# Performance work log

Measured on AMD Instinct MI355X. Metric: run time of the kernel, lower is better.

The kernel has to match this reference:

```python
import jax, jax.numpy as jnp
import numpy as np

N_NODES = 50000
N_EDGES = 800000
D_IN = 128
H1 = 128
H2 = 64
N_CLASSES = 4


def _sage_conv(x, src, dst, w_l, w_r, b, num_nodes):
    # PyG SAGEConv (aggr='mean'): out = lin_l(mean_{j->i} x_j) + lin_r(x_i)
    ones = jnp.ones((src.shape[0],), dtype=x.dtype)
    deg = jax.ops.segment_sum(ones, dst, num_segments=num_nodes)  # [N]
    agg = jax.ops.segment_sum(x[src], dst, num_segments=num_nodes)  # [N, d]
    agg = agg / jnp.maximum(deg, 1.0)[:, None]
    return agg @ w_l + b + x @ w_r


def setup_inputs() -> dict:
    key = jax.random.key(0)
    ks = jax.random.split(key, 12)
    x_content = jax.random.normal(ks[0], (N_NODES, D_IN), dtype=jnp.float32)
    edge_index = jax.random.randint(ks[1], (2, N_EDGES), 0, N_NODES, dtype=jnp.int32)
    edge_type = jax.random.randint(ks[2], (N_EDGES,), 0, 4, dtype=jnp.int32)
    s = 0.05
    params = {
        'w_l0': jax.random.normal(ks[3], (D_IN, H1), jnp.float32) * s,
        'w_r0': jax.random.normal(ks[4], (D_IN, H1), jnp.float32) * s,
        'b0': jnp.zeros((H1,), jnp.float32),
        'w_l1': jax.random.normal(ks[5], (H1, H1), jnp.float32) * s,
        'w_r1': jax.random.normal(ks[6], (H1, H1), jnp.float32) * s,
        'b1': jnp.zeros((H1,), jnp.float32),
        'w_l2': jax.random.normal(ks[7], (H1, H2), jnp.float32) * s,
        'w_r2': jax.random.normal(ks[8], (H1, H2), jnp.float32) * s,
        'b2': jnp.zeros((H2,), jnp.float32),
        'w_out': jax.random.normal(ks[9], (H2, N_CLASSES), jnp.float32) * s,
        'b_out': jnp.zeros((N_CLASSES,), jnp.float32),
    }
    return {'x_content': x_content, 'edge_index': edge_index, 'edge_type': edge_type, **params}


def reference(x_content, edge_index, edge_type,
              w_l0, w_r0, b0, w_l1, w_r1, b1, w_l2, w_r2, b2, w_out, b_out):
    # eval mode: dropout is identity
    src, dst = edge_index[0], edge_index[1]
    n = x_content.shape[0]
    x = x_content
    for (wl, wr, b) in ((w_l0, w_r0, b0), (w_l1, w_r1, b1), (w_l2, w_r2, b2)):
        x = _sage_conv(x, src, dst, wl, wr, b, n)
        x = jax.nn.relu(x)
    return x @ w_out + b_out
```

## Files before the change

### kernel.cpp

```cpp
#include <hip/hip_runtime.h>
#include <hip/hip_fp16.h>

#define D 128

constexpr int NRANGE = 8;
constexpr int NCHUNK = 32;
constexpr int RRC = 6272;

using short8 = __attribute__((ext_vector_type(8))) short;
using f32x4 = __attribute__((ext_vector_type(4))) float;

__device__ inline void splitf(float v, unsigned short& h, unsigned short& l) {
    unsigned b = __float_as_uint(v);
    h = (unsigned short)(b >> 16);
    float fh = __uint_as_float(b & 0xffff0000u);
    float r = v - fh;
    l = (unsigned short)(__float_as_uint(r) >> 16);
}


__global__ __launch_bounds__(1024) void hist_count(
    const int* __restrict__ dst, int* __restrict__ hist,
    int n_edges, int n_nodes, int rr, int ch) {
    __shared__ int lh[RRC];
    int b = blockIdx.x;
    int r = b & (NRANGE - 1), c = b >> 3;
    int t = threadIdx.x;
    for (int i = t; i < rr; i += 1024) lh[i] = 0;
    __syncthreads();
    int lo = r * rr, hi = min(n_nodes, lo + rr);
    int e0 = c * ch, e1 = min(n_edges, e0 + ch);
    for (int e = e0 + t; e < e1; e += 1024) {
        int d = dst[e];
        if (d >= lo && d < hi) atomicAdd(&lh[d - lo], 1);
    }
    __syncthreads();
    int* gh = hist + (size_t)(r * NCHUNK + c) * rr;
    for (int i = t; i < rr; i += 1024) gh[i] = lh[i];
}

__global__ __launch_bounds__(256) void deg_sum_partials(
    const int* __restrict__ hist, int* __restrict__ deg,
    int* __restrict__ partials, int n_nodes, int rr) {
    __shared__ int sd[256];
    int b = blockIdx.x, t = threadIdx.x;
    int i = b * 256 + t;
    int s = 0;
    if (i < n_nodes) {
        int r = i / rr, ii = i - r * rr;
        for (int c = 0; c < NCHUNK; ++c) s += hist[(size_t)(r * NCHUNK + c) * rr + ii];
        deg[i] = s;
    }
    sd[t] = s;
    __syncthreads();
    for (int st = 128; st > 0; st >>= 1) {
        if (t < st) sd[t] += sd[t + st];
        __syncthreads();
    }
    if (t == 0) partials[b] = sd[0];
}

__global__ __launch_bounds__(256) void scan_fill(
    const int* __restrict__ deg, const int* __restrict__ partials,
    const int* __restrict__ hist, int* __restrict__ row_ptr,
    float* __restrict__ inv_deg, int* __restrict__ base,
    int n_nodes, int rr, int nblk) {
    __shared__ int sp[256];
    __shared__ int sd[256];
    int b = blockIdx.x, t = threadIdx.x;

    sp[t] = (t < b && t < nblk) ? partials[t] : 0;
    __syncthreads();
    for (int st = 128; st > 0; st >>= 1) {
        if (t < st) sp[t] += sp[t + st];
        __syncthreads();
    }
    int pbase = sp[0];

    int i = b * 256 + t;
    int v = (i < n_nodes) ? deg[i] : 0;
    sd[t] = v;
    __syncthreads();
    for (int d = 1; d < 256; d <<= 1) {
        int x = (t >= d) ? sd[t - d] : 0;
        __syncthreads();
        sd[t] += x;
        __syncthreads();
    }
    int excl = sd[t] - v + pbase;
    if (i < n_nodes) {
        row_ptr[i] = excl;
        int dv = v > 1 ? v : 1;
        inv_deg[i] = 1.0f / (float)dv;
        if (i == n_nodes - 1) row_ptr[n_nodes] = excl + v;
        int r = i / rr, ii = i - r * rr;
        int bacc = excl;
        for (int c = 0; c < NCHUNK; ++c) {
            size_t idx = (size_t)(r * NCHUNK + c) * rr + ii;
            base[idx] = bacc;
            bacc += hist[idx];
        }
    }
}

__global__ __launch_bounds__(1024) void fill_part(
    const int* __restrict__ src, const int* __restrict__ dst,
    const int* __restrict__ base, int* __restrict__ csr,
    int n_edges, int n_nodes, int rr, int ch) {
    __shared__ int cur[RRC];
    int b = blockIdx.x;
    int r = b & (NRANGE - 1), c = b >> 3;
    int t = threadIdx.x;
    const int* gb = base + (size_t)(r * NCHUNK + c) * rr;
    for (int i = t; i < rr; i += 1024) cur[i] = gb[i];
    __syncthreads();
    int lo = r * rr, hi = min(n_nodes, lo + rr);
    int e0 = c * ch, e1 = min(n_edges, e0 + ch);
    for (int e = e0 + t; e < e1; e += 1024) {
        int d = dst[e];
        if (d >= lo && d < hi) {
            int slot = atomicAdd(&cur[d - lo], 1);
            csr[slot] = src[e];
        }
    }
}

struct WSplitArgs {
    const float* src[6];
    unsigned short* dh[6];
    unsigned short* dl[6];
    int n[6];
};

__global__ __launch_bounds__(256) void split_w(WSplitArgs a) {
    int m = blockIdx.y;
    int N = a.n[m];
    int e = blockIdx.x * 256 + threadIdx.x;
    if (e >= 128 * N) return;
    int sh = (N == 128) ? 7 : 6;
    int k = e >> sh;
    int n = e & (N - 1);
    float v = a.src[m][e];
    unsigned short h, l;
    splitf(v, h, l);
    a.dh[m][n * 128 + k] = h;
    a.dl[m][n * 128 + k] = l;
}

template <int BN, int NT, bool SPLITX>
__global__ __launch_bounds__(256) void gemm_lds(
    const float* __restrict__ X,
    const unsigned short* __restrict__ Ah, const unsigned short* __restrict__ Al,
    const unsigned short* __restrict__ W1h, const unsigned short* __restrict__ W1l,
    const unsigned short* __restrict__ W2h, const unsigned short* __restrict__ W2l,
    const float* __restrict__ bias, __half* __restrict__ P, float* __restrict__ Q, int M) {
    __shared__ short8 As[2][16 * 65];

    const int tid = threadIdx.x;
    const int wave = tid >> 6;
    const int lane = tid & 63;
    const int l15 = lane & 15;
    const int q = lane >> 4;
    const int m0 = blockIdx.x * 64;

    if constexpr (SPLITX) {
#pragma unroll
        for (int it = 0; it < 4; ++it) {
            int s = it * 256 + tid;
            int row = s >> 4, col16 = s & 15;
            int gr = min(m0 + row, M - 1);
            const float4* xp = (const float4*)X + (size_t)gr * 32 + col16 * 2;
            float4 v0 = xp[0], v1 = xp[1];
            float fv[8] = {v0.x, v0.y, v0.z, v0.w, v1.x, v1.y, v1.z, v1.w};
            short8 h, l;
#pragma unroll
            for (int j = 0; j < 8; ++j) {
                unsigned short hh_, ll_;
                splitf(fv[j], hh_, ll_);
                h[j] = (short)hh_;
                l[j] = (short)ll_;
            }
            As[0][col16 * 65 + row] = h;
            As[1][col16 * 65 + row] = l;
        }
    } else {
#pragma unroll
        for (int it = 0; it < 8; ++it) {
            int s = it * 256 + tid;
            int arr = s >> 10;
            int sp = s & 1023;
            int row = sp >> 4, col16 = sp & 15;
            int gr = min(m0 + row, M - 1);
            const unsigned short* src = (arr ? Al : Ah) + (size_t)gr * 128 + col16 * 8;
            As[arr][col16 * 65 + row] = *(const short8*)src;
        }
    }
    __syncthreads();

    const int isQ = wave >> 1;
    const int colbase = (wave & 1) * (NT * 16);
    const unsigned short* Wh = isQ ? W2h : W1h;
    const unsigned short* Wl = isQ ? W2l : W1l;

    float bvs[NT];
#pragma unroll
    for (int nt = 0; nt < NT; ++nt) bvs[nt] = isQ ? bias[colbase + nt * 16 + l15] : 0.f;

    f32x4 acc[4][NT] = {};

#pragma unroll 1
    for (int kt = 0; kt < 4; ++kt) {
        short8 Bh[NT], Bl[NT];
#pragma unroll
        for (int nt = 0; nt < NT; ++nt) {
            int c = colbase + nt * 16 + l15;
            int off = c * 128 + kt * 32 + q * 8;
            Bh[nt] = *(const short8*)(Wh + off);
            Bl[nt] = *(const short8*)(Wl + off);
        }
#pragma unroll
        for (int mt = 0; mt < 4; ++mt) {
            int ai = (kt * 4 + q) * 65 + mt * 16 + l15;
            short8 Afh = As[0][ai];
            short8 Afl = As[1][ai];
#pragma unroll
            for (int nt = 0; nt < NT; ++nt) {
                acc[mt][nt] = __builtin_amdgcn_mfma_f32_16x16x32_bf16(Afh, Bh[nt], acc[mt][nt], 0, 0, 0);
                acc[mt][nt] = __builtin_amdgcn_mfma_f32_16x16x32_bf16(Afh, Bl[nt], acc[mt][nt], 0, 0, 0);
                acc[mt][nt] = __builtin_amdgcn_mfma_f32_16x16x32_bf16(Afl, Bh[nt], acc[mt][nt], 0, 0, 0);
            }
        }
    }

#pragma unroll
    for (int mt = 0; mt < 4; ++mt) {
        int orow = m0 + mt * 16 + q * 4;
#pragma unroll
        for (int nt = 0; nt < NT; ++nt) {
            int col = colbase + nt * 16 + l15;
#pragma unroll
            for (int r = 0; r < 4; ++r) {
                int rr = orow + r;
                if (rr < M) {
                    if (isQ) Q[(size_t)rr * BN + col] = acc[mt][nt][r] + bvs[nt];
                    else P[(size_t)rr * BN + col] = __float2half(acc[mt][nt][r]);
                }
            }
        }
    }
}

__global__ __launch_bounds__(256) void agg_fused128(
    const __half* __restrict__ P, const float* __restrict__ Q,
    const int* __restrict__ row_ptr, const int* __restrict__ csr,
    const float* __restrict__ inv_deg, unsigned short* __restrict__ Hh,
    unsigned short* __restrict__ Hl, int n_nodes) {
    int node = (blockIdx.x * blockDim.x + threadIdx.x) >> 6;
    int lane = threadIdx.x & 63;
    if (node >= n_nodes) return;
    int beg = row_ptr[node], end = row_ptr[node + 1];
    const int g = lane >> 4;
    const int l = lane & 15;
    float a[2][8] = {};
    int e = beg;
    for (; e + 8 <= end; e += 8) {
#pragma unroll
        for (int j = 0; j < 2; ++j) {
            int s = csr[e + 4 * j + g];
            uint4 raw = *(const uint4*)(P + (size_t)s * 128 + l * 8);
            float2 f01 = __half22float2(*reinterpret_cast<__half2*>(&raw.x));
            float2 f23 = __half22float2(*reinterpret_cast<__half2*>(&raw.y));
            float2 f45 = __half22float2(*reinterpret_cast<__half2*>(&raw.z));
            float2 f67 = __half22float2(*reinterpret_cast<__half2*>(&raw.w));
            a[j][0] += f01.x; a[j][1] += f01.y; a[j][2] += f23.x; a[j][3] += f23.y;
            a[j][4] += f45.x; a[j][5] += f45.y; a[j][6] += f67.x; a[j][7] += f67.y;
        }
    }
    for (; e < end; e += 4) {
        int idx = e + g;
        if (idx < end) {
            int s = csr[idx];
            uint4 raw = *(const uint4*)(P + (size_t)s * 128 + l * 8);
            float2 f01 = __half22float2(*reinterpret_cast<__half2*>(&raw.x));
            float2 f23 = __half22float2(*reinterpret_cast<__half2*>(&raw.y));
            float2 f45 = __half22float2(*reinterpret_cast<__half2*>(&raw.z));
            float2 f67 = __half22float2(*reinterpret_cast<__half2*>(&raw.w));
            a[0][0] += f01.x; a[0][1] += f01.y; a[0][2] += f23.x; a[0][3] += f23.y;
            a[0][4] += f45.x; a[0][5] += f45.y; a[0][6] += f67.x; a[0][7] += f67.y;
        }
    }
    float s[8];
#pragma unroll
    for (int k = 0; k < 8; ++k) {
        s[k] = a[0][k] + a[1][k];
        s[k] += __shfl_xor(s[k], 16);
        s[k] += __shfl_xor(s[k], 32);
    }
    if (lane < 16) {
        float w = inv_deg[node];
        const float4* Q4 = (const float4*)Q;
        float4 q0 = Q4[(size_t)node * 32 + 2 * l];
        float4 q1 = Q4[(size_t)node * 32 + 2 * l + 1];
        float h0 = fmaxf(fmaf(s[0], w, q0.x), 0.f);
        float h1 = fmaxf(fmaf(s[1], w, q0.y), 0.f);
        float h2 = fmaxf(fmaf(s[2], w, q0.z), 0.f);
        float h3 = fmaxf(fmaf(s[3], w, q0.w), 0.f);
        float h4 = fmaxf(fmaf(s[4], w, q1.x), 0.f);
        float h5 = fmaxf(fmaf(s[5], w, q1.y), 0.f);
        float h6 = fmaxf(fmaf(s[6], w, q1.z), 0.f);
        float h7 = fmaxf(fmaf(s[7], w, q1.w), 0.f);
        ushort4 hv0, lv0, hv1, lv1;
        splitf(h0, hv0.x, lv0.x);
        splitf(h1, hv0.y, lv0.y);
        splitf(h2, hv0.z, lv0.z);
        splitf(h3, hv0.w, lv0.w);
        splitf(h4, hv1.x, lv1.x);
        splitf(h5, hv1.y, lv1.y);
        splitf(h6, hv1.z, lv1.z);
        splitf(h7, hv1.w, lv1.w);
        ((ushort4*)Hh)[(size_t)node * 32 + 2 * l] = hv0;
        ((ushort4*)Hh)[(size_t)node * 32 + 2 * l + 1] = hv1;
        ((ushort4*)Hl)[(size_t)node * 32 + 2 * l] = lv0;
        ((ushort4*)Hl)[(size_t)node * 32 + 2 * l + 1] = lv1;
    }
}

__global__ __launch_bounds__(256) void agg64_head(
    const __half* __restrict__ P, const float* __restrict__ Q,
    const int* __restrict__ row_ptr, const int* __restrict__ csr,
    const float* __restrict__ inv_deg, const float* __restrict__ Wo,
    const float* __restrict__ bo, float* __restrict__ out, int n_nodes) {
    int node = (blockIdx.x * blockDim.x + threadIdx.x) >> 6;
    int lane = threadIdx.x & 63;
    if (node >= n_nodes) return;
    int beg = row_ptr[node], end = row_ptr[node + 1];
    const int quarter = lane >> 4;
    const int l = lane & 15;
    float a[2][4] = {};
    int e = beg;
    for (; e + 8 <= end; e += 8) {
#pragma unroll
        for (int j = 0; j < 2; ++j) {
            int s = csr[e + 4 * j + quarter];
            uint2 raw = *(const uint2*)(P + (size_t)s * 64 + l * 4);
            float2 f01 = __half22float2(*reinterpret_cast<__half2*>(&raw.x));
            float2 f23 = __half22float2(*reinterpret_cast<__half2*>(&raw.y));
            a[j][0] += f01.x; a[j][1] += f01.y; a[j][2] += f23.x; a[j][3] += f23.y;
        }
    }
    for (; e < end; e += 4) {
        int idx = e + quarter;
        if (idx < end) {
            int s = csr[idx];
            uint2 raw = *(const uint2*)(P + (size_t)s * 64 + l * 4);
            float2 f01 = __half22float2(*reinterpret_cast<__half2*>(&raw.x));
            float2 f23 = __half22float2(*reinterpret_cast<__half2*>(&raw.y));
            a[0][0] += f01.x; a[0][1] += f01.y; a[0][2] += f23.x; a[0][3] += f23.y;
        }
    }
    float s0 = a[0][0] + a[1][0];
    float s1 = a[0][1] + a[1][1];
    float s2 = a[0][2] + a[1][2];
    float s3 = a[0][3] + a[1][3];
    s0 += __shfl_xor(s0, 16); s0 += __shfl_xor(s0, 32);
    s1 += __shfl_xor(s1, 16); s1 += __shfl_xor(s1, 32);
    s2 += __shfl_xor(s2, 16); s2 += __shfl_xor(s2, 32);
    s3 += __shfl_xor(s3, 16); s3 += __shfl_xor(s3, 32);
    if (lane < 16) {
        float w = inv_deg[node];
        float4 qv = ((const float4*)Q)[(size_t)node * 16 + l];
        float h0 = fmaxf(fmaf(s0, w, qv.x), 0.f);
        float h1 = fmaxf(fmaf(s1, w, qv.y), 0.f);
        float h2 = fmaxf(fmaf(s2, w, qv.z), 0.f);
        float h3 = fmaxf(fmaf(s3, w, qv.w), 0.f);
        const float4* Wo4 = (const float4*)Wo;
        float4 w0 = Wo4[4 * l + 0], w1 = Wo4[4 * l + 1], w2 = Wo4[4 * l + 2], w3 = Wo4[4 * l + 3];
        float c0 = h0 * w0.x + h1 * w1.x + h2 * w2.x + h3 * w3.x;
        float c1 = h0 * w0.y + h1 * w1.y + h2 * w2.y + h3 * w3.y;
        float c2 = h0 * w0.z + h1 * w1.z + h2 * w2.z + h3 * w3.z;
        float c3 = h0 * w0.w + h1 * w1.w + h2 * w2.w + h3 * w3.w;
#pragma unroll
        for (int m = 8; m > 0; m >>= 1) {
            c0 += __shfl_xor(c0, m);
            c1 += __shfl_xor(c1, m);
            c2 += __shfl_xor(c2, m);
            c3 += __shfl_xor(c3, m);
        }
        if (l == 0) {
            float4 r;
            r.x = c0 + bo[0];
            r.y = c1 + bo[1];
            r.z = c2 + bo[2];
            r.w = c3 + bo[3];
            ((float4*)out)[node] = r;
        }
    }
}

extern "C" void kernel_launch(void* const* d_in, const int* in_sizes, int n_in,
                              void* d_out, int out_size, void* d_ws, size_t ws_size,
                              hipStream_t stream) {
    const float* x = (const float*)d_in[0];
    const int* ei = (const int*)d_in[1];
    const float* wl0 = (const float*)d_in[3];
    const float* wr0 = (const float*)d_in[4];
    const float* b0 = (const float*)d_in[5];
    const float* wl1 = (const float*)d_in[6];
    const float* wr1 = (const float*)d_in[7];
    const float* b1 = (const float*)d_in[8];
    const float* wl2 = (const float*)d_in[9];
    const float* wr2 = (const float*)d_in[10];
    const float* b2 = (const float*)d_in[11];
    const float* wo = (const float*)d_in[12];
    const float* bo = (const float*)d_in[13];

    const int n_nodes = in_sizes[0] / D;
    const int n_edges = in_sizes[1] / 2;
    const int* srcp = ei;
    const int* dstp = ei + n_edges;

    char* ws = (char*)d_ws;
    size_t off = 0;
    auto carve = [&](size_t bytes) -> void* {
        void* p = ws + off;
        off = (off + bytes + 255) & ~(size_t)255;
        return p;
    };
    int* deg = (int*)carve((size_t)n_nodes * 4);
    int* row_ptr = (int*)carve((size_t)(n_nodes + 1) * 4);
    int* partials = (int*)carve(256 * 4);
    float* inv_deg = (float*)carve((size_t)n_nodes * 4);
    int* csr = (int*)carve((size_t)n_edges * 4);
    __half* Pbuf = (__half*)carve((size_t)n_nodes * D * 2);
    float* Qbuf = (float*)carve((size_t)n_nodes * D * 4);
    unsigned short* hh = (unsigned short*)carve((size_t)n_nodes * D * 2);
    unsigned short* hl = (unsigned short*)carve((size_t)n_nodes * D * 2);
    unsigned short* wt = (unsigned short*)carve((size_t)(4 * 128 * 128 + 2 * 64 * 128) * 2 * 2);
    unsigned short* wl0h = wt;
    unsigned short* wl0l = wl0h + 128 * 128;
    unsigned short* wr0h = wl0l + 128 * 128;
    unsigned short* wr0l = wr0h + 128 * 128;
    unsigned short* wl1h = wr0l + 128 * 128;
    unsigned short* wl1l = wl1h + 128 * 128;
    unsigned short* wr1h = wl1l + 128 * 128;
    unsigned short* wr1l = wr1h + 128 * 128;
    unsigned short* wl2h = wr1l + 128 * 128;
    unsigned short* wl2l = wl2h + 64 * 128;
    unsigned short* wr2h = wl2l + 64 * 128;
    unsigned short* wr2l = wr2h + 64 * 128;

    const int rr = (n_nodes + NRANGE - 1) / NRANGE;
    const int ch = (n_edges + NCHUNK - 1) / NCHUNK;
    int* hist = (int*)Qbuf;
    int* basep = (int*)Pbuf;

    const int nblk = (n_nodes + 255) / 256;

    hist_count<<<NRANGE * NCHUNK, 1024, 0, stream>>>(dstp, hist, n_edges, n_nodes, rr, ch);
    deg_sum_partials<<<nblk, 256, 0, stream>>>(hist, deg, partials, n_nodes, rr);
    scan_fill<<<nblk, 256, 0, stream>>>(deg, partials, hist, row_ptr, inv_deg, basep, n_nodes, rr, nblk);
    fill_part<<<NRANGE * NCHUNK, 1024, 0, stream>>>(srcp, dstp, basep, csr, n_edges, n_nodes, rr, ch);

    WSplitArgs wa;
    wa.src[0] = wl0; wa.dh[0] = wl0h; wa.dl[0] = wl0l; wa.n[0] = 128;
    wa.src[1] = wr0; wa.dh[1] = wr0h; wa.dl[1] = wr0l; wa.n[1] = 128;
    wa.src[2] = wl1; wa.dh[2] = wl1h; wa.dl[2] = wl1l; wa.n[2] = 128;
    wa.src[3] = wr1; wa.dh[3] = wr1h; wa.dl[3] = wr1l; wa.n[3] = 128;
    wa.src[4] = wl2; wa.dh[4] = wl2h; wa.dl[4] = wl2l; wa.n[4] = 64;
    wa.src[5] = wr2; wa.dh[5] = wr2h; wa.dl[5] = wr2l; wa.n[5] = 64;
    split_w<<<dim3(64, 6), 256, 0, stream>>>(wa);

    const int agg_blocks = (n_nodes * 64 + 255) / 256;
    const int gemm_blocks = (n_nodes + 63) / 64;

    gemm_lds<128, 4, true><<<gemm_blocks, 256, 0, stream>>>(
        x, nullptr, nullptr, wl0h, wl0l, wr0h, wr0l, b0, Pbuf, Qbuf, n_nodes);
    agg_fused128<<<agg_blocks, 256, 0, stream>>>(Pbuf, Qbuf, row_ptr, csr, inv_deg, hh, hl, n_nodes);
    gemm_lds<128, 4, false><<<gemm_blocks, 256, 0, stream>>>(
        nullptr, hh, hl, wl1h, wl1l, wr1h, wr1l, b1, Pbuf, Qbuf, n_nodes);
    agg_fused128<<<agg_blocks, 256, 0, stream>>>(Pbuf, Qbuf, row_ptr, csr, inv_deg, hh, hl, n_nodes);
    gemm_lds<64, 2, false><<<gemm_blocks, 256, 0, stream>>>(
        nullptr, hh, hl, wl2h, wl2l, wr2h, wr2l, b2, Pbuf, Qbuf, n_nodes);
    agg64_head<<<agg_blocks, 256, 0, stream>>>(Pbuf, Qbuf, row_ptr, csr, inv_deg,
                                               wo, bo, (float*)d_out, n_nodes);
}
```

Before: 306.7 us.

## Fuse neighbor aggregation into next-layer GEMM and rank-based CSR fill

The mean-aggregation kernel is fused into the following layer's split-bf16 MFMA GEMM. Each block aggregates its 64 nodes directly into LDS instead of writing hi/lo activation buffers to global memory and reading them back, and P/Q are double-buffered across layers. CSR construction now records a per-edge rank during the histogram pass using packed 16-bit LDS counters, so the fill becomes a simple per-edge scatter without a second atomic pass. The weight split is folded into the degree-sum kernel to save a launch. In exchange, the fused kernel runs only 4 waves per 64-node tile for the irregular gather, which may cut the parallelism available to hide latency.

```diff
diff --git a/kernel.cpp b/kernel.cpp
--- a/kernel.cpp
+++ b/kernel.cpp
@@ -3,9 +3,11 @@
 
 #define D 128
 
-constexpr int NRANGE = 8;
-constexpr int NCHUNK = 32;
-constexpr int RRC = 6272;
+constexpr int RSH = 14;
+constexpr int RSZ = 1 << RSH;
+constexpr int NRANGE = 4;
+constexpr int CSH = 15;
+constexpr int CSZ = 1 << CSH;
 
 using short8 = __attribute__((ext_vector_type(8))) short;
 using f32x4 = __attribute__((ext_vector_type(4))) float;
@@ -19,36 +21,62 @@
 }
 
 
-__global__ __launch_bounds__(1024) void hist_count(
-    const int* __restrict__ dst, int* __restrict__ hist,
-    int n_edges, int n_nodes, int rr, int ch) {
-    __shared__ int lh[RRC];
+__global__ __launch_bounds__(1024) void hist_rank(
+    const int* __restrict__ dst, unsigned* __restrict__ hist,
+    unsigned short* __restrict__ rank, int n_edges, int nchunk) {
+    __shared__ unsigned lh[RSZ / 2];
     int b = blockIdx.x;
-    int r = b & (NRANGE - 1), c = b >> 3;
+    int r = b & (NRANGE - 1), c = b >> 2;
     int t = threadIdx.x;
-    for (int i = t; i < rr; i += 1024) lh[i] = 0;
-    __syncthreads();
-    int lo = r * rr, hi = min(n_nodes, lo + rr);
-    int e0 = c * ch, e1 = min(n_edges, e0 + ch);
+    for (int i = t; i < RSZ / 2; i += 1024) lh[i] = 0;
+    __syncthreads();
+    int e0 = c << CSH, e1 = min(n_edges, e0 + CSZ);
     for (int e = e0 + t; e < e1; e += 1024) {
         int d = dst[e];
-        if (d >= lo && d < hi) atomicAdd(&lh[d - lo], 1);
-    }
-    __syncthreads();
-    int* gh = hist + (size_t)(r * NCHUNK + c) * rr;
-    for (int i = t; i < rr; i += 1024) gh[i] = lh[i];
-}
-
-__global__ __launch_bounds__(256) void deg_sum_partials(
-    const int* __restrict__ hist, int* __restrict__ deg,
-    int* __restrict__ partials, int n_nodes, int rr) {
+        if ((d >> RSH) == r) {
+            int ii = d & (RSZ - 1);
+            unsigned sh = (ii & 1) * 16;
+            unsigned old = atomicAdd(&lh[ii >> 1], 1u << sh);
+            rank[e] = (unsigned short)((old >> sh) & 0xffffu);
+        }
+    }
+    __syncthreads();
+    unsigned* gh = hist + (size_t)(r * nchunk + c) * (RSZ / 2);
+    for (int i = t; i < RSZ / 2; i += 1024) gh[i] = lh[i];
+}
+
+struct WSplitArgs {
+    const float* src[6];
+    unsigned short* dh[6];
+    unsigned short* dl[6];
+};
+
+__global__ __launch_bounds__(256) void deg_splitw(
+    const unsigned short* __restrict__ hist16, int* __restrict__ deg,
+    int* __restrict__ partials, int n_nodes, int nchunk, int nblk, WSplitArgs a) {
     __shared__ int sd[256];
     int b = blockIdx.x, t = threadIdx.x;
+    if (b >= nblk) {
+        int g = (b - nblk) * 256 + t;
+        int m, e, N;
+        if (g < 65536) { m = g >> 14; e = g & 16383; N = 128; }
+        else { int t2 = g - 65536; m = 4 + (t2 >> 13); e = t2 & 8191; N = 64; }
+        int sh = (N == 128) ? 7 : 6;
+        int k = e >> sh;
+        int n = e & (N - 1);
+        float v = a.src[m][e];
+        unsigned short h, l;
+        splitf(v, h, l);
+        a.dh[m][n * 128 + k] = h;
+        a.dl[m][n * 128 + k] = l;
+        return;
+    }
     int i = b * 256 + t;
     int s = 0;
     if (i < n_nodes) {
-        int r = i / rr, ii = i - r * rr;
-        for (int c = 0; c < NCHUNK; ++c) s += hist[(size_t)(r * NCHUNK + c) * rr + ii];
+        int r = i >> RSH, ii = i & (RSZ - 1);
+        const unsigned short* hp = hist16 + (size_t)r * nchunk * RSZ + ii;
+        for (int c = 0; c < nchunk; ++c) s += hp[(size_t)c * RSZ];
         deg[i] = s;
     }
     sd[t] = s;
@@ -62,9 +90,9 @@
 
 __global__ __launch_bounds__(256) void scan_fill(
     const int* __restrict__ deg, const int* __restrict__ partials,
-    const int* __restrict__ hist, int* __restrict__ row_ptr,
+    const unsigned short* __restrict__ hist16, int* __restrict__ row_ptr,
     float* __restrict__ inv_deg, int* __restrict__ base,
-    int n_nodes, int rr, int nblk) {
+    int n_nodes, int nchunk, int nblk) {
     __shared__ int sp[256];
     __shared__ int sd[256];
     int b = blockIdx.x, t = threadIdx.x;
@@ -93,64 +121,31 @@
         int dv = v > 1 ? v : 1;
         inv_deg[i] = 1.0f / (float)dv;
         if (i == n_nodes - 1) row_ptr[n_nodes] = excl + v;
-        int r = i / rr, ii = i - r * rr;
+        int r = i >> RSH, ii = i & (RSZ - 1);
         int bacc = excl;
-        for (int c = 0; c < NCHUNK; ++c) {
-            size_t idx = (size_t)(r * NCHUNK + c) * rr + ii;
+        for (int c = 0; c < nchunk; ++c) {
+            size_t idx = (size_t)(r * nchunk + c) * RSZ + ii;
             base[idx] = bacc;
-            bacc += hist[idx];
-        }
-    }
-}
-
-__global__ __launch_bounds__(1024) void fill_part(
+            bacc += hist16[idx];
+        }
+    }
+}
+
+__global__ __launch_bounds__(256) void fill_edges(
     const int* __restrict__ src, const int* __restrict__ dst,
-    const int* __restrict__ base, int* __restrict__ csr,
-    int n_edges, int n_nodes, int rr, int ch) {
-    __shared__ int cur[RRC];
-    int b = blockIdx.x;
-    int r = b & (NRANGE - 1), c = b >> 3;
-    int t = threadIdx.x;
-    const int* gb = base + (size_t)(r * NCHUNK + c) * rr;
-    for (int i = t; i < rr; i += 1024) cur[i] = gb[i];
-    __syncthreads();
-    int lo = r * rr, hi = min(n_nodes, lo + rr);
-    int e0 = c * ch, e1 = min(n_edges, e0 + ch);
-    for (int e = e0 + t; e < e1; e += 1024) {
-        int d = dst[e];
-        if (d >= lo && d < hi) {
-            int slot = atomicAdd(&cur[d - lo], 1);
-            csr[slot] = src[e];
-        }
-    }
-}
-
-struct WSplitArgs {
-    const float* src[6];
-    unsigned short* dh[6];
-    unsigned short* dl[6];
-    int n[6];
-};
-
-__global__ __launch_bounds__(256) void split_w(WSplitArgs a) {
-    int m = blockIdx.y;
-    int N = a.n[m];
+    const unsigned short* __restrict__ rank, const int* __restrict__ base,
+    int* __restrict__ csr, int n_edges, int nchunk) {
     int e = blockIdx.x * 256 + threadIdx.x;
-    if (e >= 128 * N) return;
-    int sh = (N == 128) ? 7 : 6;
-    int k = e >> sh;
-    int n = e & (N - 1);
-    float v = a.src[m][e];
-    unsigned short h, l;
-    splitf(v, h, l);
-    a.dh[m][n * 128 + k] = h;
-    a.dl[m][n * 128 + k] = l;
-}
-
-template <int BN, int NT, bool SPLITX>
-__global__ __launch_bounds__(256) void gemm_lds(
+    if (e >= n_edges) return;
+    int d = dst[e];
+    int c = e >> CSH;
+    int r = d >> RSH;
+    int slot = base[(size_t)(r * nchunk + c) * RSZ + (d & (RSZ - 1))] + rank[e];
+    csr[slot] = src[e];
+}
+
+__global__ __launch_bounds__(256) void gemm_x(
     const float* __restrict__ X,
-    const unsigned short* __restrict__ Ah, const unsigned short* __restrict__ Al,
     const unsigned short* __restrict__ W1h, const unsigned short* __restrict__ W1l,
     const unsigned short* __restrict__ W2h, const unsigned short* __restrict__ W2l,
     const float* __restrict__ bias, __half* __restrict__ P, float* __restrict__ Q, int M) {
@@ -163,36 +158,166 @@
     const int q = lane >> 4;
     const int m0 = blockIdx.x * 64;
 
-    if constexpr (SPLITX) {
-#pragma unroll
-        for (int it = 0; it < 4; ++it) {
-            int s = it * 256 + tid;
-            int row = s >> 4, col16 = s & 15;
-            int gr = min(m0 + row, M - 1);
-            const float4* xp = (const float4*)X + (size_t)gr * 32 + col16 * 2;
-            float4 v0 = xp[0], v1 = xp[1];
-            float fv[8] = {v0.x, v0.y, v0.z, v0.w, v1.x, v1.y, v1.z, v1.w};
-            short8 h, l;
-#pragma unroll
-            for (int j = 0; j < 8; ++j) {
-                unsigned short hh_, ll_;
-                splitf(fv[j], hh_, ll_);
-                h[j] = (short)hh_;
-                l[j] = (short)ll_;
-            }
-            As[0][col16 * 65 + row] = h;
-            As[1][col16 * 65 + row] = l;
-        }
-    } else {
-#pragma unroll
-        for (int it = 0; it < 8; ++it) {
-            int s = it * 256 + tid;
-            int arr = s >> 10;
-            int sp = s & 1023;
-            int row = sp >> 4, col16 = sp & 15;
-            int gr = min(m0 + row, M - 1);
-            const unsigned short* src = (arr ? Al : Ah) + (size_t)gr * 128 + col16 * 8;
-            As[arr][col16 * 65 + row] = *(const short8*)src;
+#pragma unroll
+    for (int it = 0; it < 4; ++it) {
+        int s = it * 256 + tid;
+        int row = s >> 4, col16 = s & 15;
+        int gr = min(m0 + row, M - 1);
+        const float4* xp = (const float4*)X + (size_t)gr * 32 + col16 * 2;
+        float4 v0 = xp[0], v1 = xp[1];
+        float fv[8] = {v0.x, v0.y, v0.z, v0.w, v1.x, v1.y, v1.z, v1.w};
+        short8 h, l;
+#pragma unroll
+        for (int j = 0; j < 8; ++j) {
+            unsigned short hh_, ll_;
+            splitf(fv[j], hh_, ll_);
+            h[j] = (short)hh_;
+            l[j] = (short)ll_;
+        }
+        As[0][col16 * 65 + row] = h;
+        As[1][col16 * 65 + row] = l;
+    }
+    __syncthreads();
+
+    const int isQ = wave >> 1;
+    const int colbase = (wave & 1) * 64;
+    const unsigned short* Wh = isQ ? W2h : W1h;
+    const unsigned short* Wl = isQ ? W2l : W1l;
+
+    float bvs[4];
+#pragma unroll
+    for (int nt = 0; nt < 4; ++nt) bvs[nt] = isQ ? bias[colbase + nt * 16 + l15] : 0.f;
+
+    f32x4 acc[4][4] = {};
+
+#pragma unroll 1
+    for (int kt = 0; kt < 4; ++kt) {
+        short8 Bh[4], Bl[4];
+#pragma unroll
+        for (int nt = 0; nt < 4; ++nt) {
+            int c = colbase + nt * 16 + l15;
+            int off = c * 128 + kt * 32 + q * 8;
+            Bh[nt] = *(const short8*)(Wh + off);
+            Bl[nt] = *(const short8*)(Wl + off);
+        }
+#pragma unroll
+        for (int mt = 0; mt < 4; ++mt) {
+            int ai = (kt * 4 + q) * 65 + mt * 16 + l15;
+            short8 Afh = As[0][ai];
+            short8 Afl = As[1][ai];
+#pragma unroll
+            for (int nt = 0; nt < 4; ++nt) {
+                acc[mt][nt] = __builtin_amdgcn_mfma_f32_16x16x32_bf16(Afh, Bh[nt], acc[mt][nt], 0, 0, 0);
+                acc[mt][nt] = __builtin_amdgcn_mfma_f32_16x16x32_bf16(Afh, Bl[nt], acc[mt][nt], 0, 0, 0);
+                acc[mt][nt] = __builtin_amdgcn_mfma_f32_16x16x32_bf16(Afl, Bh[nt], acc[mt][nt], 0, 0, 0);
+            }
+        }
+    }
+
+#pragma unroll
+    for (int mt = 0; mt < 4; ++mt) {
+        int orow = m0 + mt * 16 + q * 4;
+#pragma unroll
+        for (int nt = 0; nt < 4; ++nt) {
+            int col = colbase + nt * 16 + l15;
+#pragma unroll
+            for (int r = 0; r < 4; ++r) {
+                int rr = orow + r;
+                if (rr < M) {
+                    if (isQ) Q[(size_t)rr * 128 + col] = acc[mt][nt][r] + bvs[nt];
+                    else P[(size_t)rr * 128 + col] = __float2half(acc[mt][nt][r]);
+                }
+            }
+        }
+    }
+}
+
+template <int BN, int NT>
+__global__ __launch_bounds__(256) void agg_gemm(
+    const __half* __restrict__ Pprev, const float* __restrict__ Qprev,
+    const int* __restrict__ row_ptr, const int* __restrict__ csr,
+    const float* __restrict__ inv_deg,
+    const unsigned short* __restrict__ W1h, const unsigned short* __restrict__ W1l,
+    const unsigned short* __restrict__ W2h, const unsigned short* __restrict__ W2l,
+    const float* __restrict__ bias, __half* __restrict__ P, float* __restrict__ Q, int M) {
+    __shared__ short8 As[2][16 * 65];
+
+    const int tid = threadIdx.x;
+    const int wave = tid >> 6;
+    const int lane = tid & 63;
+    const int l15 = lane & 15;
+    const int q = lane >> 4;
+    const int m0 = blockIdx.x * 64;
+
+#pragma unroll 1
+    for (int i = 0; i < 16; ++i) {
+        int row = (wave << 4) + i;
+        int node = m0 + row;
+        bool valid = node < M;
+        float a[2][8] = {};
+        if (valid) {
+            int beg = row_ptr[node], end = row_ptr[node + 1];
+            int e = beg;
+            for (; e + 8 <= end; e += 8) {
+#pragma unroll
+                for (int j = 0; j < 2; ++j) {
+                    int s = csr[e + 4 * j + q];
+                    uint4 raw = *(const uint4*)(Pprev + (size_t)s * 128 + l15 * 8);
+                    float2 f01 = __half22float2(*reinterpret_cast<__half2*>(&raw.x));
+                    float2 f23 = __half22float2(*reinterpret_cast<__half2*>(&raw.y));
+                    float2 f45 = __half22float2(*reinterpret_cast<__half2*>(&raw.z));
+                    float2 f67 = __half22float2(*reinterpret_cast<__half2*>(&raw.w));
+                    a[j][0] += f01.x; a[j][1] += f01.y; a[j][2] += f23.x; a[j][3] += f23.y;
+                    a[j][4] += f45.x; a[j][5] += f45.y; a[j][6] += f67.x; a[j][7] += f67.y;
+                }
+            }
+            for (; e < end; e += 4) {
+                int idx = e + q;
+                if (idx < end) {
+                    int s = csr[idx];
+                    uint4 raw = *(const uint4*)(Pprev + (size_t)s * 128 + l15 * 8);
+                    float2 f01 = __half22float2(*reinterpret_cast<__half2*>(&raw.x));
+                    float2 f23 = __half22float2(*reinterpret_cast<__half2*>(&raw.y));
+                    float2 f45 = __half22float2(*reinterpret_cast<__half2*>(&raw.z));
+                    float2 f67 = __half22float2(*reinterpret_cast<__half2*>(&raw.w));
+                    a[0][0] += f01.x; a[0][1] += f01.y; a[0][2] += f23.x; a[0][3] += f23.y;
+                    a[0][4] += f45.x; a[0][5] += f45.y; a[0][6] += f67.x; a[0][7] += f67.y;
+                }
+            }
+        }
+        float s8[8];
+#pragma unroll
+        for (int k = 0; k < 8; ++k) {
+            s8[k] = a[0][k] + a[1][k];
+            s8[k] += __shfl_xor(s8[k], 16);
+            s8[k] += __shfl_xor(s8[k], 32);
+        }
+        if (lane < 16) {
+            short8 h8 = {}, l8 = {};
+            if (valid) {
+                float w = inv_deg[node];
+                const float4* Q4 = (const float4*)Qprev;
+                float4 q0 = Q4[(size_t)node * 32 + 2 * l15];
+                float4 q1 = Q4[(size_t)node * 32 + 2 * l15 + 1];
+                float hv[8];
+                hv[0] = fmaxf(fmaf(s8[0], w, q0.x), 0.f);
+                hv[1] = fmaxf(fmaf(s8[1], w, q0.y), 0.f);
+                hv[2] = fmaxf(fmaf(s8[2], w, q0.z), 0.f);
+                hv[3] = fmaxf(fmaf(s8[3], w, q0.w), 0.f);
+                hv[4] = fmaxf(fmaf(s8[4], w, q1.x), 0.f);
+                hv[5] = fmaxf(fmaf(s8[5], w, q1.y), 0.f);
+                hv[6] = fmaxf(fmaf(s8[6], w, q1.z), 0.f);
+                hv[7] = fmaxf(fmaf(s8[7], w, q1.w), 0.f);
+#pragma unroll
+                for (int k = 0; k < 8; ++k) {
+                    unsigned short hh_, ll_;
+                    splitf(hv[k], hh_, ll_);
+                    h8[k] = (short)hh_;
+                    l8[k] = (short)ll_;
+                }
+            }
+            As[0][l15 * 65 + row] = h8;
+            As[1][l15 * 65 + row] = l8;
         }
     }
     __syncthreads();
@@ -247,81 +372,6 @@
                 }
             }
         }
-    }
-}
-
-__global__ __launch_bounds__(256) void agg_fused128(
-    const __half* __restrict__ P, const float* __restrict__ Q,
-    const int* __restrict__ row_ptr, const int* __restrict__ csr,
-    const float* __restrict__ inv_deg, unsigned short* __restrict__ Hh,
-    unsigned short* __restrict__ Hl, int n_nodes) {
-    int node = (blockIdx.x * blockDim.x + threadIdx.x) >> 6;
-    int lane = threadIdx.x & 63;
-    if (node >= n_nodes) return;
-    int beg = row_ptr[node], end = row_ptr[node + 1];
-    const int g = lane >> 4;
-    const int l = lane & 15;
-    float a[2][8] = {};
-    int e = beg;
-    for (; e + 8 <= end; e += 8) {
-#pragma unroll
-        for (int j = 0; j < 2; ++j) {
-            int s = csr[e + 4 * j + g];
-            uint4 raw = *(const uint4*)(P + (size_t)s * 128 + l * 8);
-            float2 f01 = __half22float2(*reinterpret_cast<__half2*>(&raw.x));
-            float2 f23 = __half22float2(*reinterpret_cast<__half2*>(&raw.y));
-            float2 f45 = __half22float2(*reinterpret_cast<__half2*>(&raw.z));
-            float2 f67 = __half22float2(*reinterpret_cast<__half2*>(&raw.w));
-            a[j][0] += f01.x; a[j][1] += f01.y; a[j][2] += f23.x; a[j][3] += f23.y;
-            a[j][4] += f45.x; a[j][5] += f45.y; a[j][6] += f67.x; a[j][7] += f67.y;
-        }
-    }
-    for (; e < end; e += 4) {
-        int idx = e + g;
-        if (idx < end) {
-            int s = csr[idx];
-            uint4 raw = *(const uint4*)(P + (size_t)s * 128 + l * 8);
-            float2 f01 = __half22float2(*reinterpret_cast<__half2*>(&raw.x));
-            float2 f23 = __half22float2(*reinterpret_cast<__half2*>(&raw.y));
-            float2 f45 = __half22float2(*reinterpret_cast<__half2*>(&raw.z));
-            float2 f67 = __half22float2(*reinterpret_cast<__half2*>(&raw.w));
-            a[0][0] += f01.x; a[0][1] += f01.y; a[0][2] += f23.x; a[0][3] += f23.y;
-            a[0][4] += f45.x; a[0][5] += f45.y; a[0][6] += f67.x; a[0][7] += f67.y;
-        }
-    }
-    float s[8];
-#pragma unroll
-    for (int k = 0; k < 8; ++k) {
-        s[k] = a[0][k] + a[1][k];
-        s[k] += __shfl_xor(s[k], 16);
-        s[k] += __shfl_xor(s[k], 32);
-    }
-    if (lane < 16) {
-        float w = inv_deg[node];
-        const float4* Q4 = (const float4*)Q;
-        float4 q0 = Q4[(size_t)node * 32 + 2 * l];
-        float4 q1 = Q4[(size_t)node * 32 + 2 * l + 1];
-        float h0 = fmaxf(fmaf(s[0], w, q0.x), 0.f);
-        float h1 = fmaxf(fmaf(s[1], w, q0.y), 0.f);
-        float h2 = fmaxf(fmaf(s[2], w, q0.z), 0.f);
-        float h3 = fmaxf(fmaf(s[3], w, q0.w), 0.f);
-        float h4 = fmaxf(fmaf(s[4], w, q1.x), 0.f);
-        float h5 = fmaxf(fmaf(s[5], w, q1.y), 0.f);
-        float h6 = fmaxf(fmaf(s[6], w, q1.z), 0.f);
-        float h7 = fmaxf(fmaf(s[7], w, q1.w), 0.f);
-        ushort4 hv0, lv0, hv1, lv1;
-        splitf(h0, hv0.x, lv0.x);
-        splitf(h1, hv0.y, lv0.y);
-        splitf(h2, hv0.z, lv0.z);
-        splitf(h3, hv0.w, lv0.w);
-        splitf(h4, hv1.x, lv1.x);
-        splitf(h5, hv1.y, lv1.y);
-        splitf(h6, hv1.z, lv1.z);
-        splitf(h7, hv1.w, lv1.w);
-        ((ushort4*)Hh)[(size_t)node * 32 + 2 * l] = hv0;
-        ((ushort4*)Hh)[(size_t)node * 32 + 2 * l + 1] = hv1;
-        ((ushort4*)Hl)[(size_t)node * 32 + 2 * l] = lv0;
-        ((ushort4*)Hl)[(size_t)node * 32 + 2 * l + 1] = lv1;
     }
 }
 
@@ -430,11 +480,12 @@
     int* row_ptr = (int*)carve((size_t)(n_nodes + 1) * 4);
     int* partials = (int*)carve(256 * 4);
     float* inv_deg = (float*)carve((size_t)n_nodes * 4);
+    unsigned short* rankb = (unsigned short*)carve((size_t)n_edges * 2);
     int* csr = (int*)carve((size_t)n_edges * 4);
-    __half* Pbuf = (__half*)carve((size_t)n_nodes * D * 2);
-    float* Qbuf = (float*)carve((size_t)n_nodes * D * 4);
-    unsigned short* hh = (unsigned short*)carve((size_t)n_nodes * D * 2);
-    unsigned short* hl = (unsigned short*)carve((size_t)n_nodes * D * 2);
+    __half* Pa = (__half*)carve((size_t)n_nodes * D * 2);
+    float* Qa = (float*)carve((size_t)n_nodes * D * 4);
+    __half* Pb = (__half*)carve((size_t)n_nodes * D * 2);
+    float* Qb = (float*)carve((size_t)n_nodes * D * 4);
     unsigned short* wt = (unsigned short*)carve((size_t)(4 * 128 * 128 + 2 * 64 * 128) * 2 * 2);
     unsigned short* wl0h = wt;
     unsigned short* wl0l = wl0h + 128 * 128;
@@ -449,38 +500,37 @@
     unsigned short* wr2h = wl2l + 64 * 128;
     unsigned short* wr2l = wr2h + 64 * 128;
 
-    const int rr = (n_nodes + NRANGE - 1) / NRANGE;
-    const int ch = (n_edges + NCHUNK - 1) / NCHUNK;
-    int* hist = (int*)Qbuf;
-    int* basep = (int*)Pbuf;
+    const int nchunk = (n_edges + CSZ - 1) >> CSH;
+    unsigned* hist = (unsigned*)Qa;
+    unsigned short* hist16 = (unsigned short*)Qa;
+    int* basep = (int*)Pa;
 
     const int nblk = (n_nodes + 255) / 256;
-
-    hist_count<<<NRANGE * NCHUNK, 1024, 0, stream>>>(dstp, hist, n_edges, n_nodes, rr, ch);
-    deg_sum_partials<<<nblk, 256, 0, stream>>>(hist, deg, partials, n_nodes, rr);
-    scan_fill<<<nblk, 256, 0, stream>>>(deg, partials, hist, row_ptr, inv_deg, basep, n_nodes, rr, nblk);
-    fill_part<<<NRANGE * NCHUNK, 1024, 0, stream>>>(srcp, dstp, basep, csr, n_edges, n_nodes, rr, ch);
+    const int wblocks = (4 * 128 * 128 + 2 * 64 * 128) / 256;
 
     WSplitArgs wa;
-    wa.src[0] = wl0; wa.dh[0] = wl0h; wa.dl[0] = wl0l; wa.n[0] = 128;
-    wa.src[1] = wr0; wa.dh[1] = wr0h; wa.dl[1] = wr0l; wa.n[1] = 128;
-    wa.src[2] = wl1; wa.dh[2] = wl1h; wa.dl[2] = wl1l; wa.n[2] = 128;
-    wa.src[3] = wr1; wa.dh[3] = wr1h; wa.dl[3] = wr1l; wa.n[3] = 128;
-    wa.src[4] = wl2; wa.dh[4] = wl2h; wa.dl[4] = wl2l; wa.n[4] = 64;
-    wa.src[5] = wr2; wa.dh[5] = wr2h; wa.dl[5] = wr2l; wa.n[5] = 64;
-    split_w<<<dim3(64, 6), 256, 0, stream>>>(wa);
-
+    wa.src[0] = wl0; wa.dh[0] = wl0h; wa.dl[0] = wl0l;
+    wa.src[1] = wr0; wa.dh[1] = wr0h; wa.dl[1] = wr0l;
+    wa.src[2] = wl1; wa.dh[2] = wl1h; wa.dl[2] = wl1l;
+    wa.src[3] = wr1; wa.dh[3] = wr1h; wa.dl[3] = wr1l;
+    wa.src[4] = wl2; wa.dh[4] = wl2h; wa.dl[4] = wl2l;
+    wa.src[5] = wr2; wa.dh[5] = wr2h; wa.dl[5] = wr2l;
+
+    hist_rank<<<NRANGE * nchunk, 1024, 0, stream>>>(dstp, hist, rankb, n_edges, nchunk);
+    deg_splitw<<<nblk + wblocks, 256, 0, stream>>>(hist16, deg, partials, n_nodes, nchunk, nblk, wa);
+    scan_fill<<<nblk, 256, 0, stream>>>(deg, partials, hist16, row_ptr, inv_deg, basep,
+                                        n_nodes, nchunk, nblk);
+    fill_edges<<<(n_edges + 255) / 256, 256, 0, stream>>>(srcp, dstp, rankb, basep, csr,
+                                                          n_edges, nchunk);
+
+    const int gemm_blocks = (n_nodes + 63) / 64;
     const int agg_blocks = (n_nodes * 64 + 255) / 256;
-    const int gemm_blocks = (n_nodes + 63) / 64;
-
-    gemm_lds<128, 4, true><<<gemm_blocks, 256, 0, stream>>>(
-        x, nullptr, nullptr, wl0h, wl0l, wr0h, wr0l, b0, Pbuf, Qbuf, n_nodes);
-    agg_fused128<<<agg_blocks, 256, 0, stream>>>(Pbuf, Qbuf, row_ptr, csr, inv_deg, hh, hl, n_nodes);
-    gemm_lds<128, 4, false><<<gemm_blocks, 256, 0, stream>>>(
-        nullptr, hh, hl, wl1h, wl1l, wr1h, wr1l, b1, Pbuf, Qbuf, n_nodes);
-    agg_fused128<<<agg_blocks, 256, 0, stream>>>(Pbuf, Qbuf, row_ptr, csr, inv_deg, hh, hl, n_nodes);
-    gemm_lds<64, 2, false><<<gemm_blocks, 256, 0, stream>>>(
-        nullptr, hh, hl, wl2h, wl2l, wr2h, wr2l, b2, Pbuf, Qbuf, n_nodes);
-    agg64_head<<<agg_blocks, 256, 0, stream>>>(Pbuf, Qbuf, row_ptr, csr, inv_deg,
+
+    gemm_x<<<gemm_blocks, 256, 0, stream>>>(x, wl0h, wl0l, wr0h, wr0l, b0, Pa, Qa, n_nodes);
+    agg_gemm<128, 4><<<gemm_blocks, 256, 0, stream>>>(
+        Pa, Qa, row_ptr, csr, inv_deg, wl1h, wl1l, wr1h, wr1l, b1, Pb, Qb, n_nodes);
+    agg_gemm<64, 2><<<gemm_blocks, 256, 0, stream>>>(
+        Pb, Qb, row_ptr, csr, inv_deg, wl2h, wl2l, wr2h, wr2l, b2, Pa, (float*)Qa, n_nodes);
+    agg64_head<<<agg_blocks, 256, 0, stream>>>(Pa, (const float*)Qa, row_ptr, csr, inv_deg,
                                                wo, bo, (float*)d_out, n_nodes);
 }
```

New measurement: 366.4 us. 1.19x slower.

## Record per-edge ranks in histogram pass to make CSR fill atomic-free

Applied to the files above, without the earlier changes.

The histogram kernel now stores each edge's rank within its (range, chunk) bucket, using 16-bit counters packed two per LDS word. This lets the CSR fill run as a simple edge-parallel scatter with no second pass over dst and no shared-memory atomics. Fixed power-of-two range and chunk sizes replace the division-based partitioning, and the weight-split kernel is folded into the degree-sum launch to save one launch. The cost is an extra 2-byte-per-edge rank buffer. It also assumes fewer than 65536 nodes and per-chunk per-node counts that fit in 16 bits.

```diff
diff --git a/kernel.cpp b/kernel.cpp
--- a/kernel.cpp
+++ b/kernel.cpp
@@ -3,9 +3,11 @@
 
 #define D 128
 
-constexpr int NRANGE = 8;
-constexpr int NCHUNK = 32;
-constexpr int RRC = 6272;
+constexpr int RSH = 14;
+constexpr int RSZ = 1 << RSH;
+constexpr int NRANGE = 4;
+constexpr int CSH = 15;
+constexpr int CSZ = 1 << CSH;
 
 using short8 = __attribute__((ext_vector_type(8))) short;
 using f32x4 = __attribute__((ext_vector_type(4))) float;
@@ -19,36 +21,62 @@
 }
 
 
-__global__ __launch_bounds__(1024) void hist_count(
-    const int* __restrict__ dst, int* __restrict__ hist,
-    int n_edges, int n_nodes, int rr, int ch) {
-    __shared__ int lh[RRC];
+__global__ __launch_bounds__(1024) void hist_rank(
+    const int* __restrict__ dst, unsigned* __restrict__ hist,
+    unsigned short* __restrict__ rank, int n_edges, int nchunk) {
+    __shared__ unsigned lh[RSZ / 2];
     int b = blockIdx.x;
-    int r = b & (NRANGE - 1), c = b >> 3;
+    int r = b & (NRANGE - 1), c = b >> 2;
     int t = threadIdx.x;
-    for (int i = t; i < rr; i += 1024) lh[i] = 0;
-    __syncthreads();
-    int lo = r * rr, hi = min(n_nodes, lo + rr);
-    int e0 = c * ch, e1 = min(n_edges, e0 + ch);
+    for (int i = t; i < RSZ / 2; i += 1024) lh[i] = 0;
+    __syncthreads();
+    int e0 = c << CSH, e1 = min(n_edges, e0 + CSZ);
     for (int e = e0 + t; e < e1; e += 1024) {
         int d = dst[e];
-        if (d >= lo && d < hi) atomicAdd(&lh[d - lo], 1);
-    }
-    __syncthreads();
-    int* gh = hist + (size_t)(r * NCHUNK + c) * rr;
-    for (int i = t; i < rr; i += 1024) gh[i] = lh[i];
-}
-
-__global__ __launch_bounds__(256) void deg_sum_partials(
-    const int* __restrict__ hist, int* __restrict__ deg,
-    int* __restrict__ partials, int n_nodes, int rr) {
+        if ((d >> RSH) == r) {
+            int ii = d & (RSZ - 1);
+            unsigned sh = (ii & 1) * 16;
+            unsigned old = atomicAdd(&lh[ii >> 1], 1u << sh);
+            rank[e] = (unsigned short)((old >> sh) & 0xffffu);
+        }
+    }
+    __syncthreads();
+    unsigned* gh = hist + (size_t)(r * nchunk + c) * (RSZ / 2);
+    for (int i = t; i < RSZ / 2; i += 1024) gh[i] = lh[i];
+}
+
+struct WSplitArgs {
+    const float* src[6];
+    unsigned short* dh[6];
+    unsigned short* dl[6];
+};
+
+__global__ __launch_bounds__(256) void deg_splitw(
+    const unsigned short* __restrict__ hist16, int* __restrict__ deg,
+    int* __restrict__ partials, int n_nodes, int nchunk, int nblk, WSplitArgs a) {
     __shared__ int sd[256];
     int b = blockIdx.x, t = threadIdx.x;
+    if (b >= nblk) {
+        int g = (b - nblk) * 256 + t;
+        int m, e, N;
+        if (g < 65536) { m = g >> 14; e = g & 16383; N = 128; }
+        else { int t2 = g - 65536; m = 4 + (t2 >> 13); e = t2 & 8191; N = 64; }
+        int sh = (N == 128) ? 7 : 6;
+        int k = e >> sh;
+        int n = e & (N - 1);
+        float v = a.src[m][e];
+        unsigned short h, l;
+        splitf(v, h, l);
+        a.dh[m][n * 128 + k] = h;
+        a.dl[m][n * 128 + k] = l;
+        return;
+    }
     int i = b * 256 + t;
     int s = 0;
     if (i < n_nodes) {
-        int r = i / rr, ii = i - r * rr;
-        for (int c = 0; c < NCHUNK; ++c) s += hist[(size_t)(r * NCHUNK + c) * rr + ii];
+        int r = i >> RSH, ii = i & (RSZ - 1);
+        const unsigned short* hp = hist16 + (size_t)r * nchunk * RSZ + ii;
+        for (int c = 0; c < nchunk; ++c) s += hp[(size_t)c * RSZ];
         deg[i] = s;
     }
     sd[t] = s;
@@ -62,9 +90,9 @@
 
 __global__ __launch_bounds__(256) void scan_fill(
     const int* __restrict__ deg, const int* __restrict__ partials,
-    const int* __restrict__ hist, int* __restrict__ row_ptr,
+    const unsigned short* __restrict__ hist16, int* __restrict__ row_ptr,
     float* __restrict__ inv_deg, int* __restrict__ base,
-    int n_nodes, int rr, int nblk) {
+    int n_nodes, int nchunk, int nblk) {
     __shared__ int sp[256];
     __shared__ int sd[256];
     int b = blockIdx.x, t = threadIdx.x;
@@ -93,58 +121,27 @@
         int dv = v > 1 ? v : 1;
         inv_deg[i] = 1.0f / (float)dv;
         if (i == n_nodes - 1) row_ptr[n_nodes] = excl + v;
-        int r = i / rr, ii = i - r * rr;
+        int r = i >> RSH, ii = i & (RSZ - 1);
         int bacc = excl;
-        for (int c = 0; c < NCHUNK; ++c) {
-            size_t idx = (size_t)(r * NCHUNK + c) * rr + ii;
+        for (int c = 0; c < nchunk; ++c) {
+            size_t idx = (size_t)(r * nchunk + c) * RSZ + ii;
             base[idx] = bacc;
-            bacc += hist[idx];
-        }
-    }
-}
-
-__global__ __launch_bounds__(1024) void fill_part(
+            bacc += hist16[idx];
+        }
+    }
+}
+
+__global__ __launch_bounds__(256) void fill_edges(
     const int* __restrict__ src, const int* __restrict__ dst,
-    const int* __restrict__ base, int* __restrict__ csr,
-    int n_edges, int n_nodes, int rr, int ch) {
-    __shared__ int cur[RRC];
-    int b = blockIdx.x;
-    int r = b & (NRANGE - 1), c = b >> 3;
-    int t = threadIdx.x;
-    const int* gb = base + (size_t)(r * NCHUNK + c) * rr;
-    for (int i = t; i < rr; i += 1024) cur[i] = gb[i];
-    __syncthreads();
-    int lo = r * rr, hi = min(n_nodes, lo + rr);
-    int e0 = c * ch, e1 = min(n_edges, e0 + ch);
-    for (int e = e0 + t; e < e1; e += 1024) {
-        int d = dst[e];
-        if (d >= lo && d < hi) {
-            int slot = atomicAdd(&cur[d - lo], 1);
-            csr[slot] = src[e];
-        }
-    }
-}
-
-struct WSplitArgs {
-    const float* src[6];
-    unsigned short* dh[6];
-    unsigned short* dl[6];
-    int n[6];
-};
-
-__global__ __launch_bounds__(256) void split_w(WSplitArgs a) {
-    int m = blockIdx.y;
-    int N = a.n[m];
+    const unsigned short* __restrict__ rank, const int* __restrict__ base,
+    int* __restrict__ csr, int n_edges, int nchunk) {
     int e = blockIdx.x * 256 + threadIdx.x;
-    if (e >= 128 * N) return;
-    int sh = (N == 128) ? 7 : 6;
-    int k = e >> sh;
-    int n = e & (N - 1);
-    float v = a.src[m][e];
-    unsigned short h, l;
-    splitf(v, h, l);
-    a.dh[m][n * 128 + k] = h;
-    a.dl[m][n * 128 + k] = l;
+    if (e >= n_edges) return;
+    int d = dst[e];
+    int c = e >> CSH;
+    int r = d >> RSH;
+    int slot = base[(size_t)(r * nchunk + c) * RSZ + (d & (RSZ - 1))] + rank[e];
+    csr[slot] = src[e];
 }
 
 template <int BN, int NT, bool SPLITX>
@@ -430,6 +427,7 @@
     int* row_ptr = (int*)carve((size_t)(n_nodes + 1) * 4);
     int* partials = (int*)carve(256 * 4);
     float* inv_deg = (float*)carve((size_t)n_nodes * 4);
+    unsigned short* rankb = (unsigned short*)carve((size_t)n_edges * 2);
     int* csr = (int*)carve((size_t)n_edges * 4);
     __half* Pbuf = (__half*)carve((size_t)n_nodes * D * 2);
     float* Qbuf = (float*)carve((size_t)n_nodes * D * 4);
@@ -449,26 +447,28 @@
     unsigned short* wr2h = wl2l + 64 * 128;
     unsigned short* wr2l = wr2h + 64 * 128;
 
-    const int rr = (n_nodes + NRANGE - 1) / NRANGE;
-    const int ch = (n_edges + NCHUNK - 1) / NCHUNK;
-    int* hist = (int*)Qbuf;
+    const int nchunk = (n_edges + CSZ - 1) >> CSH;
+    unsigned* hist = (unsigned*)Qbuf;
+    unsigned short* hist16 = (unsigned short*)Qbuf;
     int* basep = (int*)Pbuf;
 
     const int nblk = (n_nodes + 255) / 256;
-
-    hist_count<<<NRANGE * NCHUNK, 1024, 0, stream>>>(dstp, hist, n_edges, n_nodes, rr, ch);
-    deg_sum_partials<<<nblk, 256, 0, stream>>>(hist, deg, partials, n_nodes, rr);
-    scan_fill<<<nblk, 256, 0, stream>>>(deg, partials, hist, row_ptr, inv_deg, basep, n_nodes, rr, nblk);
-    fill_part<<<NRANGE * NCHUNK, 1024, 0, stream>>>(srcp, dstp, basep, csr, n_edges, n_nodes, rr, ch);
+    const int wblocks = (4 * 128 * 128 + 2 * 64 * 128) / 256;
 
     WSplitArgs wa;
-    wa.src[0] = wl0; wa.dh[0] = wl0h; wa.dl[0] = wl0l; wa.n[0] = 128;
-    wa.src[1] = wr0; wa.dh[1] = wr0h; wa.dl[1] = wr0l; wa.n[1] = 128;
-    wa.src[2] = wl1; wa.dh[2] = wl1h; wa.dl[2] = wl1l; wa.n[2] = 128;
-    wa.src[3] = wr1; wa.dh[3] = wr1h; wa.dl[3] = wr1l; wa.n[3] = 128;
-    wa.src[4] = wl2; wa.dh[4] = wl2h; wa.dl[4] = wl2l; wa.n[4] = 64;
-    wa.src[5] = wr2; wa.dh[5] = wr2h; wa.dl[5] = wr2l; wa.n[5] = 64;
-    split_w<<<dim3(64, 6), 256, 0, stream>>>(wa);
+    wa.src[0] = wl0; wa.dh[0] = wl0h; wa.dl[0] = wl0l;
+    wa.src[1] = wr0; wa.dh[1] = wr0h; wa.dl[1] = wr0l;
+    wa.src[2] = wl1; wa.dh[2] = wl1h; wa.dl[2] = wl1l;
+    wa.src[3] = wr1; wa.dh[3] = wr1h; wa.dl[3] = wr1l;
+    wa.src[4] = wl2; wa.dh[4] = wl2h; wa.dl[4] = wl2l;
+    wa.src[5] = wr2; wa.dh[5] = wr2h; wa.dl[5] = wr2l;
+
+    hist_rank<<<NRANGE * nchunk, 1024, 0, stream>>>(dstp, hist, rankb, n_edges, nchunk);
+    deg_splitw<<<nblk + wblocks, 256, 0, stream>>>(hist16, deg, partials, n_nodes, nchunk, nblk, wa);
+    scan_fill<<<nblk, 256, 0, stream>>>(deg, partials, hist16, row_ptr, inv_deg, basep,
+                                        n_nodes, nchunk, nblk);
+    fill_edges<<<(n_edges + 255) / 256, 256, 0, stream>>>(srcp, dstp, rankb, basep, csr,
+                                                          n_edges, nchunk);
 
     const int agg_blocks = (n_nodes * 64 + 255) / 256;
     const int gemm_blocks = (n_nodes + 63) / 64;
```

After: 306.5 us. Within noise of the previous version (-0.1%).
